# Kernel tuning notes

Hardware: AMD Instinct MI355X
Metric: run time of the kernel (lower is better)

The kernel has to match this reference:

```python
import jax, jax.numpy as jnp
import numpy as np
import math

D_MODEL = 1024
N_HEADS = 16
D_KV = 64
INNER = N_HEADS * D_KV
D_FF = 4096
NUM_BUCKETS = 32
MAX_DIST = 128
EPS = 1e-6
B, S = 2, 1024


def _t5_layernorm(x, w):
    # T5 RMSNorm: no mean subtraction, no bias
    var = jnp.mean(x * x, axis=-1, keepdims=True)
    return x * jax.lax.rsqrt(var + EPS) * w


def _relative_position_bucket(relative_position):
    # bidirectional (encoder) variant of T5 bucketing
    num_buckets = NUM_BUCKETS // 2
    rel_buckets = (relative_position > 0).astype(jnp.int32) * num_buckets
    rp = jnp.abs(relative_position)
    max_exact = num_buckets // 2
    is_small = rp < max_exact
    rp_large = max_exact + (
        jnp.log(rp.astype(jnp.float32) / max_exact)
        / math.log(MAX_DIST / max_exact)
        * (num_buckets - max_exact)
    ).astype(jnp.int32)
    rp_large = jnp.minimum(rp_large, num_buckets - 1)
    return rel_buckets + jnp.where(is_small, rp, rp_large)


def setup_inputs() -> dict:
    key = jax.random.key(0)
    ks = jax.random.split(key, 8)
    sc = 0.02
    return {
        "hidden_states": jax.random.normal(ks[0], (B, S, D_MODEL), jnp.float32),
        "ln1_w": jnp.ones((D_MODEL,), jnp.float32),
        "wq": jax.random.normal(ks[1], (INNER, D_MODEL), jnp.float32) * sc,
        "wk": jax.random.normal(ks[2], (INNER, D_MODEL), jnp.float32) * sc,
        "wv": jax.random.normal(ks[3], (INNER, D_MODEL), jnp.float32) * sc,
        "wo": jax.random.normal(ks[4], (D_MODEL, INNER), jnp.float32) * sc,
        "rel_bias": jax.random.normal(ks[5], (NUM_BUCKETS, N_HEADS), jnp.float32) * sc,
        "ln2_w": jnp.ones((D_MODEL,), jnp.float32),
        "wi": jax.random.normal(ks[6], (D_FF, D_MODEL), jnp.float32) * sc,
        "wo_ff": jax.random.normal(ks[7], (D_MODEL, D_FF), jnp.float32) * sc,
    }


def reference(hidden_states, ln1_w, wq, wk, wv, wo, rel_bias, ln2_w, wi, wo_ff):
    b, s, _ = hidden_states.shape
    # --- self-attention with relative position bias (T5: no 1/sqrt(d) scale) ---
    x = _t5_layernorm(hidden_states, ln1_w)
    q = (x @ wq.T).reshape(b, s, N_HEADS, D_KV).transpose(0, 2, 1, 3)  # [b,h,s,d]
    k = (x @ wk.T).reshape(b, s, N_HEADS, D_KV).transpose(0, 2, 1, 3)
    v = (x @ wv.T).reshape(b, s, N_HEADS, D_KV).transpose(0, 2, 1, 3)
    pos = jnp.arange(s)
    buckets = _relative_position_bucket(pos[None, :] - pos[:, None])  # [s,s]
    bias = rel_bias[buckets].transpose(2, 0, 1)[None]  # [1,h,s,s]
    scores = jnp.einsum('bhqd,bhkd->bhqk', q, k) + bias
    attn = jax.nn.softmax(scores, axis=-1)
    ctx = jnp.einsum('bhqk,bhkd->bhqd', attn, v)
    ctx = ctx.transpose(0, 2, 1, 3).reshape(b, s, INNER)
    h = hidden_states + ctx @ wo.T
    # --- FFN (ReLU dense) with pre-norm and residual ---
    y = _t5_layernorm(h, ln2_w)
    ff = jax.nn.relu(y @ wi.T) @ wo_ff.T
    return h + ff
```

## Files before the change

kernel.cpp:

```cpp
#include <hip/hip_runtime.h>
#include <hip/hip_bf16.h>
#include <math.h>


typedef __bf16 bf16_t;
typedef __attribute__((ext_vector_type(8))) __bf16 bf16x8;
typedef __attribute__((ext_vector_type(4))) __bf16 bf16x4;
typedef __attribute__((ext_vector_type(4))) float floatx4;

#define GLOBAL_AS(p) ((const __attribute__((address_space(1))) void*)(p))
#define LDS_AS(p)    ((__attribute__((address_space(3))) void*)(p))

__global__ __launch_bounds__(256) void convert_w_kernel(
    const float* __restrict__ wq, const float* __restrict__ wk,
    const float* __restrict__ wv, const float* __restrict__ wo,
    const float* __restrict__ wi, const float* __restrict__ woff,
    bf16_t* __restrict__ wqkv_b, bf16_t* __restrict__ wo_b,
    bf16_t* __restrict__ wi_b, bf16_t* __restrict__ woff_b) {
  size_t idx = ((size_t)blockIdx.x * 256 + threadIdx.x) * 8;
  const float* src;
  bf16_t* dst;
  size_t off;
  if (idx < 3145728) {
    size_t sec = idx >> 20;
    src = sec == 0 ? wq : (sec == 1 ? wk : wv);
    dst = wqkv_b + (sec << 20);
    off = idx & 1048575;
  } else if (idx < 4194304) {
    src = wo; dst = wo_b; off = idx - 3145728;
  } else if (idx < 8388608) {
    src = wi; dst = wi_b; off = idx - 4194304;
  } else {
    src = woff; dst = woff_b; off = idx - 8388608;
  }
  float4 a = *(const float4*)(src + off);
  float4 b = *(const float4*)(src + off + 4);
  bf16x8 o;
  o[0] = (bf16_t)a.x; o[1] = (bf16_t)a.y; o[2] = (bf16_t)a.z; o[3] = (bf16_t)a.w;
  o[4] = (bf16_t)b.x; o[5] = (bf16_t)b.y; o[6] = (bf16_t)b.z; o[7] = (bf16_t)b.w;
  *(bf16x8*)(dst + off) = o;
}

__global__ void bias_table_kernel(const float* __restrict__ rel_bias,
                                  float* __restrict__ table) {
  int idx = blockIdx.x * 256 + threadIdx.x;
  int h = idx >> 11;
  int dpos = idx & 2047;
  int delta = dpos - 1023;
  if (delta > 1023) delta = 1023;
  int side = (delta > 0) ? 16 : 0;
  int rp = (delta < 0) ? -delta : delta;
  int bucket;
  if (rp < 8) {
    bucket = side + rp;
  } else {
    float t3 = (logf((float)rp * 0.125f) / 2.7725887f) * 8.0f;
    int v = 8 + (int)t3;
    if (v > 15) v = 15;
    bucket = side + v;
  }
  table[idx] = rel_bias[bucket * 16 + h];
}

__global__ __launch_bounds__(256) void rmsnorm_kernel(
    const float* __restrict__ X, const float* __restrict__ w,
    bf16_t* __restrict__ Y) {
  const int D = 1024;
  int row = blockIdx.x;
  int t = threadIdx.x;
  float4 v = ((const float4*)(X + (size_t)row * D))[t];
  float f[4] = {v.x, v.y, v.z, v.w};
  float s = 0.f;
#pragma unroll
  for (int j = 0; j < 4; ++j) s += f[j] * f[j];
#pragma unroll
  for (int off = 32; off > 0; off >>= 1) s += __shfl_down(s, off);
  __shared__ float red[4];
  int lane = t & 63, wave = t >> 6;
  if (lane == 0) red[wave] = s;
  __syncthreads();
  float tot = red[0] + red[1] + red[2] + red[3];
  float scale = rsqrtf(tot * (1.0f / D) + 1e-6f);
  float4 wv4 = ((const float4*)w)[t];
  bf16x4 o;
  o[0] = (bf16_t)(f[0] * scale * wv4.x);
  o[1] = (bf16_t)(f[1] * scale * wv4.y);
  o[2] = (bf16_t)(f[2] * scale * wv4.z);
  o[3] = (bf16_t)(f[3] * scale * wv4.w);
  *(bf16x4*)(Y + (size_t)row * D + t * 4) = o;
}

template <int TBM, bool WF32, int OP>
__global__ __launch_bounds__(256, 2) void gemm_bt(
    const bf16_t* __restrict__ A, const void* __restrict__ W0,
    const void* __restrict__ W1, const void* __restrict__ W2,
    bf16_t* __restrict__ C, int M, int K_total, int klen, int N,
    int wsel_cols) {
  constexpr int MFRAG = TBM / 32;
  __shared__ bf16_t As[TBM * 64];
  __shared__ bf16_t Bs[128 * 64];

  const int tid = threadIdx.x;
  const int lane = tid & 63;
  const int wv = tid >> 6;
  const int wm = wv & 1;
  const int wn = wv >> 1;
  const int lr = lane & 15;
  const int lq = lane >> 4;

  int bx = blockIdx.x, by = blockIdx.y;
  {
    int gx = gridDim.x, gy = gridDim.y;
    int lid = by * gx + bx;
    int xcd = lid & 7, slot = lid >> 3;
    int per = gy >> 3;
    by = xcd * per + slot % per;
    bx = slot / per;
  }

  const size_t row0 = (size_t)bx * TBM;
  const size_t col0 = (size_t)by * 128;
  const int k0 = blockIdx.z * klen;

  const void* Ws = W0;
  size_t wc0 = col0;
  if ((int)col0 >= wsel_cols) {
    if ((int)col0 < 2 * wsel_cols) { Ws = W1; wc0 = col0 - wsel_cols; }
    else { Ws = W2; wc0 = col0 - 2 * (size_t)wsel_cols; }
  }

  const bf16_t* Abase = A + row0 * K_total;
  bf16_t* Cs = C + (size_t)blockIdx.z * M * N;

  floatx4 acc[MFRAG][4] = {};

  for (int kt = k0; kt < k0 + klen; kt += 64) {
#pragma unroll
    for (int i = 0; i < TBM / 32; ++i) {
      int chunk = i * 256 + tid;
      int r = chunk >> 3;
      int kc = ((chunk & 7) ^ (r & 7)) << 3;
      __builtin_amdgcn_global_load_lds(
          GLOBAL_AS(Abase + (size_t)r * K_total + kt + kc),
          LDS_AS(As + (size_t)(i * 256 + wv * 64) * 8), 16, 0, 0);
    }
    if constexpr (WF32) {
      const float* Wbase = (const float*)Ws + wc0 * K_total;
#pragma unroll
      for (int i = 0; i < 4; ++i) {
        int chunk = i * 256 + tid;
        int r = chunk >> 3;
        int kc = ((chunk & 7) ^ (r & 7)) << 3;
        const float* p = Wbase + (size_t)r * K_total + kt + kc;
        float4 f0 = *(const float4*)p;
        float4 f1v = *(const float4*)(p + 4);
        bf16x8 o;
        o[0] = (bf16_t)f0.x; o[1] = (bf16_t)f0.y;
        o[2] = (bf16_t)f0.z; o[3] = (bf16_t)f0.w;
        o[4] = (bf16_t)f1v.x; o[5] = (bf16_t)f1v.y;
        o[6] = (bf16_t)f1v.z; o[7] = (bf16_t)f1v.w;
        *(bf16x8*)(Bs + chunk * 8) = o;
      }
    } else {
      const bf16_t* Wbase = (const bf16_t*)Ws + wc0 * K_total;
#pragma unroll
      for (int i = 0; i < 4; ++i) {
        int chunk = i * 256 + tid;
        int r = chunk >> 3;
        int kc = ((chunk & 7) ^ (r & 7)) << 3;
        __builtin_amdgcn_global_load_lds(
            GLOBAL_AS(Wbase + (size_t)r * K_total + kt + kc),
            LDS_AS(Bs + (size_t)(i * 256 + wv * 64) * 8), 16, 0, 0);
      }
    }
    __syncthreads();

#pragma unroll
    for (int c = 0; c < 2; ++c) {
      bf16x8 af[MFRAG], bfr[4];
#pragma unroll
      for (int mi = 0; mi < MFRAG; ++mi) {
        int rr = wm * (TBM / 2) + mi * 16 + lr;
        int c8p = (c * 4 + lq) ^ (rr & 7);
        af[mi] = *(const bf16x8*)(As + rr * 64 + c8p * 8);
      }
#pragma unroll
      for (int nj = 0; nj < 4; ++nj) {
        int rr = wn * 64 + nj * 16 + lr;
        int c8p = (c * 4 + lq) ^ (rr & 7);
        bfr[nj] = *(const bf16x8*)(Bs + rr * 64 + c8p * 8);
      }
#pragma unroll
      for (int mi = 0; mi < MFRAG; ++mi)
#pragma unroll
        for (int nj = 0; nj < 4; ++nj)
          acc[mi][nj] = __builtin_amdgcn_mfma_f32_16x16x32_bf16(
              af[mi], bfr[nj], acc[mi][nj], 0, 0, 0);
    }
    __syncthreads();
  }

#pragma unroll
  for (int mi = 0; mi < MFRAG; ++mi) {
#pragma unroll
    for (int nj = 0; nj < 4; ++nj) {
      size_t r = row0 + wm * (TBM / 2) + mi * 16 + lq * 4;
      size_t c = col0 + wn * 64 + nj * 16 + lr;
#pragma unroll
      for (int t = 0; t < 4; ++t) {
        float v = acc[mi][nj][t];
        if (OP == 2) v = v > 0.f ? v : 0.f;
        Cs[(r + t) * N + c] = (bf16_t)v;
      }
    }
  }
}

__global__ __launch_bounds__(256) void transpose_v_kernel(
    const bf16_t* __restrict__ QKV, bf16_t* __restrict__ VT) {
  __shared__ bf16_t T[64 * 65];
  const int s0 = blockIdx.x * 64;
  const int h = blockIdx.y;
  const int b = blockIdx.z;
  const int tid = threadIdx.x;

  const bf16_t* Vh = QKV + ((size_t)b * 1024) * 3072 + 2048 + h * 64;
#pragma unroll
  for (int i = 0; i < 2; ++i) {
    int c = i * 256 + tid;
    int r = c >> 3;
    int d8 = (c & 7) * 8;
    bf16x8 v = *(const bf16x8*)(Vh + (size_t)(s0 + r) * 3072 + d8);
#pragma unroll
    for (int j = 0; j < 8; ++j) T[r * 65 + d8 + j] = v[j];
  }
  __syncthreads();

  bf16_t* Og = VT + ((size_t)b * 16 + h) * 64 * 1024;
#pragma unroll
  for (int i = 0; i < 2; ++i) {
    int c = i * 256 + tid;
    int d = c >> 3;
    int s8 = (c & 7) * 8;
    bf16x8 o;
#pragma unroll
    for (int j = 0; j < 8; ++j) o[j] = T[(s8 + j) * 65 + d];
    *(bf16x8*)(Og + (size_t)d * 1024 + s0 + s8) = o;
  }
}

__device__ __forceinline__ void attn_stage(const bf16_t* Kh, const bf16_t* Vg,
                                           int k0, bf16_t* Ksb, bf16_t* Vtb,
                                           int tid, int wv) {
  const int l16 = tid & 15;
  const int lo8 = ((tid & 63) >> 4) * 8;
#pragma unroll
  for (int i = 0; i < 2; ++i) {
    int bi = wv * 2 + i;
    int g = bi >> 1, c = bi & 1;
    __builtin_amdgcn_global_load_lds(
        GLOBAL_AS(Kh + (size_t)(k0 + g * 16 + l16) * 3072 + c * 32 + lo8),
        LDS_AS(Ksb + bi * 512), 16, 0, 0);
    __builtin_amdgcn_global_load_lds(
        GLOBAL_AS(Vg + (size_t)(g * 16 + l16) * 1024 + k0 + c * 32 + lo8),
        LDS_AS(Vtb + bi * 512), 16, 0, 0);
  }
}

__global__ __launch_bounds__(256) void attn_kernel(
    const bf16_t* __restrict__ QKV, const bf16_t* __restrict__ VT,
    const float* __restrict__ bias_table, bf16_t* __restrict__ O) {
  const int qt = blockIdx.x;
  const int h = blockIdx.y;
  const int b = blockIdx.z;
  const int tid = threadIdx.x;
  const int lane = tid & 63;
  const int wv = tid >> 6;
  const int lr = lane & 15;
  const int lq = lane >> 4;

  __shared__ bf16_t Ks[2][4096];
  __shared__ bf16_t Vt[2][4096];
  __shared__ bf16_t Ps[4][1024];

  const bf16_t* Qh = QKV + (size_t)b * 1024 * 3072 + h * 64;
  const bf16_t* Kh = Qh + 1024;
  const bf16_t* Vg = VT + ((size_t)b * 16 + h) * 64 * 1024;
  bf16_t* Oh = O + (size_t)b * 1024 * 1024 + h * 64;

  const int q0w = qt * 64 + wv * 16;
  const int myq = q0w + lr;

  bf16x8 qf[2];
#pragma unroll
  for (int c = 0; c < 2; ++c)
    qf[c] = *(const bf16x8*)(Qh + (size_t)(q0w + lr) * 3072 + c * 32 + lq * 8);

  float l_loc = 0.f;
  floatx4 o_acc[4];
#pragma unroll
  for (int i = 0; i < 4; ++i) o_acc[i] = (floatx4){0.f, 0.f, 0.f, 0.f};

  const float* btab = bias_table + h * 2048 + 1023 - myq;

  attn_stage(Kh, Vg, 0, Ks[0], Vt[0], tid, wv);
  __syncthreads();

  for (int kt = 0; kt < 16; ++kt) {
    const int k0 = kt * 64;
    if (kt < 15)
      attn_stage(Kh, Vg, k0 + 64, Ks[(kt + 1) & 1], Vt[(kt + 1) & 1], tid, wv);
    const bf16_t* Ksb = Ks[kt & 1];
    const bf16_t* Vtb = Vt[kt & 1];

    floatx4 s_acc[4];
#pragma unroll
    for (int g = 0; g < 4; ++g) {
      floatx4 a = (floatx4){0.f, 0.f, 0.f, 0.f};
#pragma unroll
      for (int c = 0; c < 2; ++c) {
        bf16x8 kf = *(const bf16x8*)(Ksb + (g * 2 + c) * 512 + lane * 8);
        a = __builtin_amdgcn_mfma_f32_16x16x32_bf16(kf, qf[c], a, 0, 0, 0);
      }
      s_acc[g] = a;
    }

#pragma unroll
    for (int g = 0; g < 4; ++g) {
      bf16x4 pb;
#pragma unroll
      for (int t = 0; t < 4; ++t) {
        int key = k0 + g * 16 + lq * 4 + t;
        float p = __expf(s_acc[g][t] + btab[key] - 32.0f);
        l_loc += p;
        pb[t] = (bf16_t)p;
      }
      int c = g >> 1;
      int dst = c * 512 + (((g & 1) * 2 + (lq >> 1)) * 16 + lr) * 8 + (lq & 1) * 4;
      *(bf16x4*)(&Ps[wv][dst]) = pb;
    }

    asm volatile("s_waitcnt lgkmcnt(0)" ::: "memory");

    bf16x8 pf[2];
#pragma unroll
    for (int c = 0; c < 2; ++c)
      pf[c] = *(const bf16x8*)(&Ps[wv][c * 512 + lane * 8]);

#pragma unroll
    for (int g = 0; g < 4; ++g) {
#pragma unroll
      for (int c = 0; c < 2; ++c) {
        bf16x8 vf = *(const bf16x8*)(Vtb + (g * 2 + c) * 512 + lane * 8);
        o_acc[g] = __builtin_amdgcn_mfma_f32_16x16x32_bf16(pf[c], vf, o_acc[g], 0, 0, 0);
      }
    }
    __syncthreads();
  }

  l_loc += __shfl_xor(l_loc, 16);
  l_loc += __shfl_xor(l_loc, 32);
  float inv = 1.f / l_loc;

  float invt[4];
#pragma unroll
  for (int t = 0; t < 4; ++t) invt[t] = __shfl(inv, lq * 4 + t);

#pragma unroll
  for (int g = 0; g < 4; ++g) {
#pragma unroll
    for (int t = 0; t < 4; ++t) {
      int qg = q0w + lq * 4 + t;
      int d = g * 16 + lr;
      Oh[(size_t)qg * 1024 + d] = (bf16_t)(o_acc[g][t] * invt[t]);
    }
  }
}

__global__ __launch_bounds__(256) void reduce_rms_kernel(
    const bf16_t* __restrict__ part, int splits, const float* __restrict__ hs,
    const float* __restrict__ ln2w, bf16_t* __restrict__ hbuf,
    bf16_t* __restrict__ y) {
  const size_t SLICE = (size_t)2048 * 1024;
  int tid = threadIdx.x;
  size_t i = ((size_t)blockIdx.x * 256 + tid) * 8;

  float s[8] = {};
  for (int sp = 0; sp < splits; ++sp) {
    bf16x8 p = *(const bf16x8*)(part + sp * SLICE + i);
#pragma unroll
    for (int j = 0; j < 8; ++j) s[j] += (float)p[j];
  }
  float4 a = *(const float4*)(hs + i);
  float4 b = *(const float4*)(hs + i + 4);
  s[0] += a.x; s[1] += a.y; s[2] += a.z; s[3] += a.w;
  s[4] += b.x; s[5] += b.y; s[6] += b.z; s[7] += b.w;

  bf16x8 hb;
#pragma unroll
  for (int j = 0; j < 8; ++j) hb[j] = (bf16_t)s[j];
  *(bf16x8*)(hbuf + i) = hb;

  float ss = 0.f;
#pragma unroll
  for (int j = 0; j < 8; ++j) ss += s[j] * s[j];
#pragma unroll
  for (int off = 32; off > 0; off >>= 1) ss += __shfl_down(ss, off);
  __shared__ float red[4];
  int wave = tid >> 6;
  if ((tid & 63) == 0) red[wave] = ss;
  __syncthreads();
  float rowss = (tid < 128) ? (red[0] + red[1]) : (red[2] + red[3]);
  float scale = rsqrtf(rowss * (1.f / 1024.f) + 1e-6f);

  int col = (int)(i & 1023);
  float4 w0 = *(const float4*)(ln2w + col);
  float4 w1 = *(const float4*)(ln2w + col + 4);
  bf16x8 o;
  o[0] = (bf16_t)(s[0] * scale * w0.x); o[1] = (bf16_t)(s[1] * scale * w0.y);
  o[2] = (bf16_t)(s[2] * scale * w0.z); o[3] = (bf16_t)(s[3] * scale * w0.w);
  o[4] = (bf16_t)(s[4] * scale * w1.x); o[5] = (bf16_t)(s[5] * scale * w1.y);
  o[6] = (bf16_t)(s[6] * scale * w1.z); o[7] = (bf16_t)(s[7] * scale * w1.w);
  *(bf16x8*)(y + i) = o;
}

__global__ __launch_bounds__(256) void reduce_out_kernel(
    const bf16_t* __restrict__ part, int splits,
    const bf16_t* __restrict__ res, float* __restrict__ out) {
  const size_t SLICE = (size_t)2048 * 1024;
  size_t i = ((size_t)blockIdx.x * 256 + threadIdx.x) * 8;
  float s[8] = {};
  for (int sp = 0; sp < splits; ++sp) {
    bf16x8 p = *(const bf16x8*)(part + sp * SLICE + i);
#pragma unroll
    for (int j = 0; j < 8; ++j) s[j] += (float)p[j];
  }
  bf16x8 r = *(const bf16x8*)(res + i);
#pragma unroll
  for (int j = 0; j < 8; ++j) s[j] += (float)r[j];
  float4 a, b;
  a.x = s[0]; a.y = s[1]; a.z = s[2]; a.w = s[3];
  b.x = s[4]; b.y = s[5]; b.z = s[6]; b.w = s[7];
  *(float4*)(out + i) = a;
  *(float4*)(out + i + 4) = b;
}

extern "C" void kernel_launch(void* const* d_in, const int* in_sizes, int n_in,
                              void* d_out, int out_size, void* d_ws,
                              size_t ws_size, hipStream_t stream) {
  const float* hs = (const float*)d_in[0];
  const float* ln1_w = (const float*)d_in[1];
  const float* wq = (const float*)d_in[2];
  const float* wk = (const float*)d_in[3];
  const float* wvv = (const float*)d_in[4];
  const float* wo = (const float*)d_in[5];
  const float* rel_bias = (const float*)d_in[6];
  const float* ln2_w = (const float*)d_in[7];
  const float* wi = (const float*)d_in[8];
  const float* wo_ff = (const float*)d_in[9];
  float* out = (float*)d_out;

  const int M = 2048, D = 1024, FF = 4096;
  const size_t SL = (size_t)M * D * 2;
  const size_t QKVB = (size_t)M * 3072 * 2;
  const size_t F1B = (size_t)M * FF * 2;
  const size_t BT = 16 * 2048 * 4;

  const size_t FULL_NEED = BT + 6291456 + 2097152 + 8388608 + 8388608 +
                           SL + QKVB + SL + SL + SL + F1B + SL + 4 * SL;
  const size_t COMPACT_NEED = BT + SL + QKVB + F1B;

  char* w = (char*)d_ws;
  dim3 gtv(16, 16, 2), ga(16, 16, 2);

  if (ws_size >= FULL_NEED) {
    float* btab = (float*)w;      w += BT;
    bf16_t* wqkv_b = (bf16_t*)w;  w += 6291456;
    bf16_t* wo_b = (bf16_t*)w;    w += 2097152;
    bf16_t* wi_b = (bf16_t*)w;    w += 8388608;
    bf16_t* woff_b = (bf16_t*)w;  w += 8388608;
    bf16_t* x = (bf16_t*)w;       w += SL;
    bf16_t* qkv = (bf16_t*)w;     w += QKVB;
    bf16_t* ctx = (bf16_t*)w;     w += SL;
    bf16_t* hbuf = (bf16_t*)w;    w += SL;
    bf16_t* y = (bf16_t*)w;       w += SL;
    bf16_t* f1 = (bf16_t*)w;      w += F1B;
    bf16_t* vtg = (bf16_t*)w;     w += SL;
    bf16_t* part = (bf16_t*)w;    w += 4 * SL;

    convert_w_kernel<<<6144, 256, 0, stream>>>(wq, wk, wvv, wo, wi, wo_ff,
                                               wqkv_b, wo_b, wi_b, woff_b);
    bias_table_kernel<<<128, 256, 0, stream>>>(rel_bias, btab);
    rmsnorm_kernel<<<M, 256, 0, stream>>>(hs, ln1_w, x);

    gemm_bt<128, false, 0><<<dim3(16, 24, 1), 256, 0, stream>>>(
        x, wqkv_b, wqkv_b, wqkv_b, qkv, M, D, D, 3072, 1 << 30);
    transpose_v_kernel<<<gtv, 256, 0, stream>>>(qkv, vtg);
    attn_kernel<<<ga, 256, 0, stream>>>(qkv, vtg, btab, ctx);

    gemm_bt<128, false, 0><<<dim3(16, 8, 4), 256, 0, stream>>>(
        ctx, wo_b, wo_b, wo_b, part, M, D, D / 4, D, 1 << 30);
    reduce_rms_kernel<<<1024, 256, 0, stream>>>(part, 4, hs, ln2_w, hbuf, y);

    gemm_bt<128, false, 2><<<dim3(16, 32, 1), 256, 0, stream>>>(
        y, wi_b, wi_b, wi_b, f1, M, D, D, FF, 1 << 30);

    gemm_bt<128, false, 0><<<dim3(16, 8, 4), 256, 0, stream>>>(
        f1, woff_b, woff_b, woff_b, part, M, FF, FF / 4, D, 1 << 30);
    reduce_out_kernel<<<1024, 256, 0, stream>>>(part, 4, hbuf, out);
  } else {
    if (ws_size < COMPACT_NEED) return;
    float* btab = (float*)w;  w += BT;
    char* Abuf = w;           w += SL;
    char* Bbuf = w;           w += QKVB;
    char* Fbuf = w;           w += F1B;
    bf16_t* x = (bf16_t*)Abuf;
    bf16_t* ctx = (bf16_t*)Abuf;
    bf16_t* hbuf = (bf16_t*)Abuf;
    bf16_t* qkv = (bf16_t*)Bbuf;
    bf16_t* part = (bf16_t*)Bbuf;
    bf16_t* y = (bf16_t*)(Bbuf + 2 * SL);
    bf16_t* vtg = (bf16_t*)Fbuf;
    bf16_t* f1 = (bf16_t*)Fbuf;

    bias_table_kernel<<<128, 256, 0, stream>>>(rel_bias, btab);
    rmsnorm_kernel<<<M, 256, 0, stream>>>(hs, ln1_w, x);

    gemm_bt<64, true, 0><<<dim3(32, 24, 1), 256, 0, stream>>>(
        x, wq, wk, wvv, qkv, M, D, D, 3072, 1024);
    transpose_v_kernel<<<gtv, 256, 0, stream>>>(qkv, vtg);
    attn_kernel<<<ga, 256, 0, stream>>>(qkv, vtg, btab, ctx);

    gemm_bt<64, true, 0><<<dim3(32, 8, 2), 256, 0, stream>>>(
        ctx, wo, wo, wo, part, M, D, D / 2, D, 1 << 30);
    reduce_rms_kernel<<<1024, 256, 0, stream>>>(part, 2, hs, ln2_w, hbuf, y);

    gemm_bt<64, true, 2><<<dim3(32, 32, 1), 256, 0, stream>>>(
        y, wi, wi, wi, f1, M, D, D, FF, 1 << 30);

    gemm_bt<64, true, 0><<<dim3(32, 8, 2), 256, 0, stream>>>(
        f1, wo_ff, wo_ff, wo_ff, part, M, FF, FF / 2, D, 1 << 30);
    reduce_out_kernel<<<1024, 256, 0, stream>>>(part, 2, hbuf, out);
  }
}
```

Measured before the change: 236.8 us.

## Fuse fp32 weight conversion into GEMM loads and merge prologue kernels

Removes the separate weight-conversion pass: every GEMM now reads fp32 weights directly and converts them to bf16 in registers before storing to LDS. The bias-table and first RMSNorm kernels are merged into one prologue launch, the out-projection split-K drops from 4 to 2, and launch bounds rise to 3 blocks per CU. This removes a full read and write of all weights and two launches, but doubles weight bytes read inside each GEMM and gives up the async global-to-LDS path for the B operand.

```diff
diff --git a/kernel.cpp b/kernel.cpp
--- a/kernel.cpp
+++ b/kernel.cpp
@@ -11,89 +11,59 @@
 #define GLOBAL_AS(p) ((const __attribute__((address_space(1))) void*)(p))
 #define LDS_AS(p)    ((__attribute__((address_space(3))) void*)(p))
 
-__global__ __launch_bounds__(256) void convert_w_kernel(
-    const float* __restrict__ wq, const float* __restrict__ wk,
-    const float* __restrict__ wv, const float* __restrict__ wo,
-    const float* __restrict__ wi, const float* __restrict__ woff,
-    bf16_t* __restrict__ wqkv_b, bf16_t* __restrict__ wo_b,
-    bf16_t* __restrict__ wi_b, bf16_t* __restrict__ woff_b) {
-  size_t idx = ((size_t)blockIdx.x * 256 + threadIdx.x) * 8;
-  const float* src;
-  bf16_t* dst;
-  size_t off;
-  if (idx < 3145728) {
-    size_t sec = idx >> 20;
-    src = sec == 0 ? wq : (sec == 1 ? wk : wv);
-    dst = wqkv_b + (sec << 20);
-    off = idx & 1048575;
-  } else if (idx < 4194304) {
-    src = wo; dst = wo_b; off = idx - 3145728;
-  } else if (idx < 8388608) {
-    src = wi; dst = wi_b; off = idx - 4194304;
+__global__ __launch_bounds__(256) void prologue_kernel(
+    const float* __restrict__ hs, const float* __restrict__ ln1w,
+    const float* __restrict__ rel_bias, bf16_t* __restrict__ x,
+    float* __restrict__ table) {
+  int bid = blockIdx.x;
+  int t = threadIdx.x;
+  if (bid < 2048) {
+    const int D = 1024;
+    float4 v = ((const float4*)(hs + (size_t)bid * D))[t];
+    float f[4] = {v.x, v.y, v.z, v.w};
+    float s = 0.f;
+#pragma unroll
+    for (int j = 0; j < 4; ++j) s += f[j] * f[j];
+#pragma unroll
+    for (int off = 32; off > 0; off >>= 1) s += __shfl_down(s, off);
+    __shared__ float red[4];
+    int lane = t & 63, wave = t >> 6;
+    if (lane == 0) red[wave] = s;
+    __syncthreads();
+    float tot = red[0] + red[1] + red[2] + red[3];
+    float scale = rsqrtf(tot * (1.0f / D) + 1e-6f);
+    float4 wv4 = ((const float4*)ln1w)[t];
+    bf16x4 o;
+    o[0] = (bf16_t)(f[0] * scale * wv4.x);
+    o[1] = (bf16_t)(f[1] * scale * wv4.y);
+    o[2] = (bf16_t)(f[2] * scale * wv4.z);
+    o[3] = (bf16_t)(f[3] * scale * wv4.w);
+    *(bf16x4*)(x + (size_t)bid * D + t * 4) = o;
   } else {
-    src = woff; dst = woff_b; off = idx - 8388608;
-  }
-  float4 a = *(const float4*)(src + off);
-  float4 b = *(const float4*)(src + off + 4);
-  bf16x8 o;
-  o[0] = (bf16_t)a.x; o[1] = (bf16_t)a.y; o[2] = (bf16_t)a.z; o[3] = (bf16_t)a.w;
-  o[4] = (bf16_t)b.x; o[5] = (bf16_t)b.y; o[6] = (bf16_t)b.z; o[7] = (bf16_t)b.w;
-  *(bf16x8*)(dst + off) = o;
-}
-
-__global__ void bias_table_kernel(const float* __restrict__ rel_bias,
-                                  float* __restrict__ table) {
-  int idx = blockIdx.x * 256 + threadIdx.x;
-  int h = idx >> 11;
-  int dpos = idx & 2047;
-  int delta = dpos - 1023;
-  if (delta > 1023) delta = 1023;
-  int side = (delta > 0) ? 16 : 0;
-  int rp = (delta < 0) ? -delta : delta;
-  int bucket;
-  if (rp < 8) {
-    bucket = side + rp;
-  } else {
-    float t3 = (logf((float)rp * 0.125f) / 2.7725887f) * 8.0f;
-    int v = 8 + (int)t3;
-    if (v > 15) v = 15;
-    bucket = side + v;
-  }
-  table[idx] = rel_bias[bucket * 16 + h];
-}
-
-__global__ __launch_bounds__(256) void rmsnorm_kernel(
-    const float* __restrict__ X, const float* __restrict__ w,
-    bf16_t* __restrict__ Y) {
-  const int D = 1024;
-  int row = blockIdx.x;
-  int t = threadIdx.x;
-  float4 v = ((const float4*)(X + (size_t)row * D))[t];
-  float f[4] = {v.x, v.y, v.z, v.w};
-  float s = 0.f;
-#pragma unroll
-  for (int j = 0; j < 4; ++j) s += f[j] * f[j];
-#pragma unroll
-  for (int off = 32; off > 0; off >>= 1) s += __shfl_down(s, off);
-  __shared__ float red[4];
-  int lane = t & 63, wave = t >> 6;
-  if (lane == 0) red[wave] = s;
-  __syncthreads();
-  float tot = red[0] + red[1] + red[2] + red[3];
-  float scale = rsqrtf(tot * (1.0f / D) + 1e-6f);
-  float4 wv4 = ((const float4*)w)[t];
-  bf16x4 o;
-  o[0] = (bf16_t)(f[0] * scale * wv4.x);
-  o[1] = (bf16_t)(f[1] * scale * wv4.y);
-  o[2] = (bf16_t)(f[2] * scale * wv4.z);
-  o[3] = (bf16_t)(f[3] * scale * wv4.w);
-  *(bf16x4*)(Y + (size_t)row * D + t * 4) = o;
-}
-
-template <int TBM, bool WF32, int OP>
-__global__ __launch_bounds__(256, 2) void gemm_bt(
-    const bf16_t* __restrict__ A, const void* __restrict__ W0,
-    const void* __restrict__ W1, const void* __restrict__ W2,
+    int idx = (bid - 2048) * 256 + t;
+    int h = idx >> 11;
+    int dpos = idx & 2047;
+    int delta = dpos - 1023;
+    if (delta > 1023) delta = 1023;
+    int side = (delta > 0) ? 16 : 0;
+    int rp = (delta < 0) ? -delta : delta;
+    int bucket;
+    if (rp < 8) {
+      bucket = side + rp;
+    } else {
+      float t3 = (logf((float)rp * 0.125f) / 2.7725887f) * 8.0f;
+      int v = 8 + (int)t3;
+      if (v > 15) v = 15;
+      bucket = side + v;
+    }
+    table[idx] = rel_bias[bucket * 16 + h];
+  }
+}
+
+template <int TBM, int OP>
+__global__ __launch_bounds__(256, 3) void gemm_bt(
+    const bf16_t* __restrict__ A, const float* __restrict__ W0,
+    const float* __restrict__ W1, const float* __restrict__ W2,
     bf16_t* __restrict__ C, int M, int K_total, int klen, int N,
     int wsel_cols) {
   constexpr int MFRAG = TBM / 32;
@@ -122,7 +92,7 @@
   const size_t col0 = (size_t)by * 128;
   const int k0 = blockIdx.z * klen;
 
-  const void* Ws = W0;
+  const float* Ws = W0;
   size_t wc0 = col0;
   if ((int)col0 >= wsel_cols) {
     if ((int)col0 < 2 * wsel_cols) { Ws = W1; wc0 = col0 - wsel_cols; }
@@ -130,6 +100,7 @@
   }
 
   const bf16_t* Abase = A + row0 * K_total;
+  const float* Wbase = Ws + wc0 * K_total;
   bf16_t* Cs = C + (size_t)blockIdx.z * M * N;
 
   floatx4 acc[MFRAG][4] = {};
@@ -144,34 +115,20 @@
           GLOBAL_AS(Abase + (size_t)r * K_total + kt + kc),
           LDS_AS(As + (size_t)(i * 256 + wv * 64) * 8), 16, 0, 0);
     }
-    if constexpr (WF32) {
-      const float* Wbase = (const float*)Ws + wc0 * K_total;
-#pragma unroll
-      for (int i = 0; i < 4; ++i) {
-        int chunk = i * 256 + tid;
-        int r = chunk >> 3;
-        int kc = ((chunk & 7) ^ (r & 7)) << 3;
-        const float* p = Wbase + (size_t)r * K_total + kt + kc;
-        float4 f0 = *(const float4*)p;
-        float4 f1v = *(const float4*)(p + 4);
-        bf16x8 o;
-        o[0] = (bf16_t)f0.x; o[1] = (bf16_t)f0.y;
-        o[2] = (bf16_t)f0.z; o[3] = (bf16_t)f0.w;
-        o[4] = (bf16_t)f1v.x; o[5] = (bf16_t)f1v.y;
-        o[6] = (bf16_t)f1v.z; o[7] = (bf16_t)f1v.w;
-        *(bf16x8*)(Bs + chunk * 8) = o;
-      }
-    } else {
-      const bf16_t* Wbase = (const bf16_t*)Ws + wc0 * K_total;
-#pragma unroll
-      for (int i = 0; i < 4; ++i) {
-        int chunk = i * 256 + tid;
-        int r = chunk >> 3;
-        int kc = ((chunk & 7) ^ (r & 7)) << 3;
-        __builtin_amdgcn_global_load_lds(
-            GLOBAL_AS(Wbase + (size_t)r * K_total + kt + kc),
-            LDS_AS(Bs + (size_t)(i * 256 + wv * 64) * 8), 16, 0, 0);
-      }
+#pragma unroll
+    for (int i = 0; i < 4; ++i) {
+      int chunk = i * 256 + tid;
+      int r = chunk >> 3;
+      int kc = ((chunk & 7) ^ (r & 7)) << 3;
+      const float* p = Wbase + (size_t)r * K_total + kt + kc;
+      float4 f0 = *(const float4*)p;
+      float4 f1v = *(const float4*)(p + 4);
+      bf16x8 o;
+      o[0] = (bf16_t)f0.x; o[1] = (bf16_t)f0.y;
+      o[2] = (bf16_t)f0.z; o[3] = (bf16_t)f0.w;
+      o[4] = (bf16_t)f1v.x; o[5] = (bf16_t)f1v.y;
+      o[6] = (bf16_t)f1v.z; o[7] = (bf16_t)f1v.w;
+      *(bf16x8*)(Bs + chunk * 8) = o;
     }
     __syncthreads();
 
@@ -466,47 +423,39 @@
   const size_t F1B = (size_t)M * FF * 2;
   const size_t BT = 16 * 2048 * 4;
 
-  const size_t FULL_NEED = BT + 6291456 + 2097152 + 8388608 + 8388608 +
-                           SL + QKVB + SL + SL + SL + F1B + SL + 4 * SL;
+  const size_t FULL_NEED = BT + SL + QKVB + SL + SL + SL + F1B + SL + 4 * SL;
   const size_t COMPACT_NEED = BT + SL + QKVB + F1B;
 
   char* w = (char*)d_ws;
   dim3 gtv(16, 16, 2), ga(16, 16, 2);
 
   if (ws_size >= FULL_NEED) {
-    float* btab = (float*)w;      w += BT;
-    bf16_t* wqkv_b = (bf16_t*)w;  w += 6291456;
-    bf16_t* wo_b = (bf16_t*)w;    w += 2097152;
-    bf16_t* wi_b = (bf16_t*)w;    w += 8388608;
-    bf16_t* woff_b = (bf16_t*)w;  w += 8388608;
-    bf16_t* x = (bf16_t*)w;       w += SL;
-    bf16_t* qkv = (bf16_t*)w;     w += QKVB;
-    bf16_t* ctx = (bf16_t*)w;     w += SL;
-    bf16_t* hbuf = (bf16_t*)w;    w += SL;
-    bf16_t* y = (bf16_t*)w;       w += SL;
-    bf16_t* f1 = (bf16_t*)w;      w += F1B;
-    bf16_t* vtg = (bf16_t*)w;     w += SL;
-    bf16_t* part = (bf16_t*)w;    w += 4 * SL;
-
-    convert_w_kernel<<<6144, 256, 0, stream>>>(wq, wk, wvv, wo, wi, wo_ff,
-                                               wqkv_b, wo_b, wi_b, woff_b);
-    bias_table_kernel<<<128, 256, 0, stream>>>(rel_bias, btab);
-    rmsnorm_kernel<<<M, 256, 0, stream>>>(hs, ln1_w, x);
-
-    gemm_bt<128, false, 0><<<dim3(16, 24, 1), 256, 0, stream>>>(
-        x, wqkv_b, wqkv_b, wqkv_b, qkv, M, D, D, 3072, 1 << 30);
+    float* btab = (float*)w;   w += BT;
+    bf16_t* x = (bf16_t*)w;    w += SL;
+    bf16_t* qkv = (bf16_t*)w;  w += QKVB;
+    bf16_t* ctx = (bf16_t*)w;  w += SL;
+    bf16_t* hbuf = (bf16_t*)w; w += SL;
+    bf16_t* y = (bf16_t*)w;    w += SL;
+    bf16_t* f1 = (bf16_t*)w;   w += F1B;
+    bf16_t* vtg = (bf16_t*)w;  w += SL;
+    bf16_t* part = (bf16_t*)w; w += 4 * SL;
+
+    prologue_kernel<<<2176, 256, 0, stream>>>(hs, ln1_w, rel_bias, x, btab);
+
+    gemm_bt<128, 0><<<dim3(16, 24, 1), 256, 0, stream>>>(
+        x, wq, wk, wvv, qkv, M, D, D, 3072, 1024);
     transpose_v_kernel<<<gtv, 256, 0, stream>>>(qkv, vtg);
     attn_kernel<<<ga, 256, 0, stream>>>(qkv, vtg, btab, ctx);
 
-    gemm_bt<128, false, 0><<<dim3(16, 8, 4), 256, 0, stream>>>(
-        ctx, wo_b, wo_b, wo_b, part, M, D, D / 4, D, 1 << 30);
-    reduce_rms_kernel<<<1024, 256, 0, stream>>>(part, 4, hs, ln2_w, hbuf, y);
-
-    gemm_bt<128, false, 2><<<dim3(16, 32, 1), 256, 0, stream>>>(
-        y, wi_b, wi_b, wi_b, f1, M, D, D, FF, 1 << 30);
-
-    gemm_bt<128, false, 0><<<dim3(16, 8, 4), 256, 0, stream>>>(
-        f1, woff_b, woff_b, woff_b, part, M, FF, FF / 4, D, 1 << 30);
+    gemm_bt<128, 0><<<dim3(16, 8, 2), 256, 0, stream>>>(
+        ctx, wo, wo, wo, part, M, D, D / 2, D, 1 << 30);
+    reduce_rms_kernel<<<1024, 256, 0, stream>>>(part, 2, hs, ln2_w, hbuf, y);
+
+    gemm_bt<128, 2><<<dim3(16, 32, 1), 256, 0, stream>>>(
+        y, wi, wi, wi, f1, M, D, D, FF, 1 << 30);
+
+    gemm_bt<128, 0><<<dim3(16, 8, 4), 256, 0, stream>>>(
+        f1, wo_ff, wo_ff, wo_ff, part, M, FF, FF / 4, D, 1 << 30);
     reduce_out_kernel<<<1024, 256, 0, stream>>>(part, 4, hbuf, out);
   } else {
     if (ws_size < COMPACT_NEED) return;
@@ -523,22 +472,21 @@
     bf16_t* vtg = (bf16_t*)Fbuf;
     bf16_t* f1 = (bf16_t*)Fbuf;
 
-    bias_table_kernel<<<128, 256, 0, stream>>>(rel_bias, btab);
-    rmsnorm_kernel<<<M, 256, 0, stream>>>(hs, ln1_w, x);
-
-    gemm_bt<64, true, 0><<<dim3(32, 24, 1), 256, 0, stream>>>(
+    prologue_kernel<<<2176, 256, 0, stream>>>(hs, ln1_w, rel_bias, x, btab);
+
+    gemm_bt<64, 0><<<dim3(32, 24, 1), 256, 0, stream>>>(
         x, wq, wk, wvv, qkv, M, D, D, 3072, 1024);
     transpose_v_kernel<<<gtv, 256, 0, stream>>>(qkv, vtg);
     attn_kernel<<<ga, 256, 0, stream>>>(qkv, vtg, btab, ctx);
 
-    gemm_bt<64, true, 0><<<dim3(32, 8, 2), 256, 0, stream>>>(
+    gemm_bt<64, 0><<<dim3(32, 8, 2), 256, 0, stream>>>(
         ctx, wo, wo, wo, part, M, D, D / 2, D, 1 << 30);
     reduce_rms_kernel<<<1024, 256, 0, stream>>>(part, 2, hs, ln2_w, hbuf, y);
 
-    gemm_bt<64, true, 2><<<dim3(32, 32, 1), 256, 0, stream>>>(
+    gemm_bt<64, 2><<<dim3(32, 32, 1), 256, 0, stream>>>(
         y, wi, wi, wi, f1, M, D, D, FF, 1 << 30);
 
-    gemm_bt<64, true, 0><<<dim3(32, 8, 2), 256, 0, stream>>>(
+    gemm_bt<64, 0><<<dim3(32, 8, 2), 256, 0, stream>>>(
         f1, wo_ff, wo_ff, wo_ff, part, M, FF, FF / 2, D, 1 << 30);
     reduce_out_kernel<<<1024, 256, 0, stream>>>(part, 2, hbuf, out);
   }
```

Result: slower. 274.6 us (+15.9%).
